# Kernel tuning notes

Measured on AMD Instinct MI355X. Metric: run time of the kernel, lower is better.

The kernel has to match this reference:

```python
import jax, jax.numpy as jnp
import numpy as np

_SCAN_CHUNK = 32


def _causal_decay_scan(x, decay, init):
    """Inclusive scan out[t] = decay*out[t-1] + x[t], chunked closed form.
    x: [B,H,T,D], decay: [1,H,1], init: [B,H,D]. Returns [B,H,T,D]."""
    B, H, T, D = x.shape
    C = min(_SCAN_CHUNK, T)
    assert T % C == 0
    nC = T // C
    log_decay = jnp.log(jnp.clip(decay.astype(jnp.float32), 1e-8, None))  # [1,H,1]
    c_idx = jnp.arange(C, dtype=jnp.float32)
    log_p = log_decay[..., None] * c_idx.reshape(1, 1, C, 1)              # [1,H,C,1]
    p = jnp.exp(log_p)
    inv_p = jnp.exp(-log_p)
    init_p = jnp.exp(log_decay[..., None] * (c_idx + 1.0).reshape(1, 1, C, 1))
    # [nC, B, H, C, D] so lax.scan chains chunk states causally
    xc = x.reshape(B, H, nC, C, D).transpose(2, 0, 1, 3, 4).astype(jnp.float32)

    def step(state, chunk):  # state [B,H,D], chunk [B,H,C,D]
        cs = jnp.cumsum(chunk * inv_p, axis=2)
        out = cs * p + state[:, :, None, :] * init_p
        return out[:, :, -1, :], out

    _, outs = jax.lax.scan(step, init.astype(jnp.float32), xc)
    return outs.transpose(1, 2, 0, 3, 4).reshape(B, H, T, D).astype(x.dtype)


def _phi(x):
    return jax.nn.elu(x) + 1.0


def setup_inputs() -> dict:
    key = jax.random.key(0)
    ks = jax.random.split(key, 5)
    B, T, hidden, H = 4, 4096, 1024, 16
    s = 1.0 / np.sqrt(hidden)
    x = jax.random.normal(ks[0], (B, T, hidden), dtype=jnp.float32)
    Wqkv = jax.random.normal(ks[1], (3 * hidden, hidden), dtype=jnp.float32) * s
    Wout = jax.random.normal(ks[2], (hidden, hidden), dtype=jnp.float32) * s
    Wgate = jax.random.normal(ks[3], (hidden, hidden), dtype=jnp.float32) * s
    bgate = jnp.zeros((hidden,), dtype=jnp.float32)
    logit = float(np.log(0.95 / 0.05))  # sigmoid(logit) == 0.95
    decay_param = jnp.full((H,), logit, dtype=jnp.float32)
    return {"x": x, "Wqkv": Wqkv, "Wout": Wout, "Wgate": Wgate,
            "bgate": bgate, "decay_param": decay_param}


def reference(x, Wqkv, Wout, Wgate, bgate, decay_param):
    B, T, hidden = x.shape
    H = decay_param.shape[0]
    D = hidden // H
    qkv = x @ Wqkv.T                       # [B,T,3*hidden]
    q, k, v = jnp.split(qkv, 3, axis=-1)
    # [B,T,hidden] -> [B,H,T,D]
    q = q.reshape(B, T, H, D).transpose(0, 2, 1, 3)
    k = k.reshape(B, T, H, D).transpose(0, 2, 1, 3)
    v = v.reshape(B, T, H, D).transpose(0, 2, 1, 3)
    q = _phi(q)
    k = _phi(k)
    decay = jax.nn.sigmoid(decay_param).reshape(1, H, 1)
    kv_init = jnp.zeros((B, H, D), dtype=x.dtype)
    ksum_init = jnp.zeros((B, H, D), dtype=x.dtype)
    running_kv = _causal_decay_scan(k * v, decay, kv_init)
    running_ksum = _causal_decay_scan(k, decay, ksum_init)
    den = jnp.clip(jnp.sum(q * running_ksum, axis=-1, keepdims=True), 1e-6, None)
    out = q * running_kv / den             # [B,H,T,D]
    v_direct = v.transpose(0, 2, 1, 3).reshape(B, T, hidden)
    out = out.transpose(0, 2, 1, 3).reshape(B, T, hidden)
    g = jax.nn.sigmoid(out @ Wgate.T + bgate)
    out = g * out + (1.0 - g) * v_direct
    return out @ Wout.T
```

## Files before the change

### kernel.cpp

```cpp
#include <hip/hip_runtime.h>

typedef unsigned short u16;
typedef __bf16 bf16x8 __attribute__((ext_vector_type(8)));
typedef float f32x4 __attribute__((ext_vector_type(4)));

#define BB 4
#define TT 4096
#define HID 1024
#define NH 16
#define HD 64
#define BT (BB*TT)
#define NCH 128
#define LOG_NCH 7
#define CLEN (TT/NCH)

__device__ __forceinline__ float bf2f(u16 u) {
    return __uint_as_float(((unsigned)u) << 16);
}
__device__ __forceinline__ u16 f2bf(float f) {
    unsigned u = __float_as_uint(f);
    unsigned r = 0x7FFFu + ((u >> 16) & 1u);
    return (u16)((u + r) >> 16);
}
__device__ __forceinline__ float phi(float x) {
    return x > 0.f ? x + 1.f : __expf(x);
}
__device__ __forceinline__ float sigmoidf(float x) {
    return 1.f / (1.f + __expf(-x));
}
__device__ __forceinline__ float4 u4_to_f4(ushort4 u) {
    return make_float4(bf2f(u.x), bf2f(u.y), bf2f(u.z), bf2f(u.w));
}

#define CN1 (BT*HID/4)
#define CN2 (3*HID*HID/4)
#define CN3 (HID*HID/4)
#define CN4 (HID*HID/4)
__global__ void convert_all(const float4* __restrict__ x,    const float4* __restrict__ wqkv,
                            const float4* __restrict__ wgate, const float4* __restrict__ wout,
                            ushort4* __restrict__ xb,    ushort4* __restrict__ wqkvb,
                            ushort4* __restrict__ wgateb, ushort4* __restrict__ woutb) {
    int i = blockIdx.x * 256 + threadIdx.x;
    const float4* src; ushort4* dst; int j;
    if (i < CN1)                 { src = x;     dst = xb;     j = i; }
    else if (i < CN1+CN2)        { src = wqkv;  dst = wqkvb;  j = i - CN1; }
    else if (i < CN1+CN2+CN3)    { src = wgate; dst = wgateb; j = i - CN1 - CN2; }
    else                         { src = wout;  dst = woutb;  j = i - CN1 - CN2 - CN3; }
    float4 f = src[j];
    ushort4 u;
    u.x = f2bf(f.x); u.y = f2bf(f.y); u.z = f2bf(f.z); u.w = f2bf(f.w);
    dst[j] = u;
}

template<int EPI>
__global__ __launch_bounds__(512, 2)
void gemm256(const u16* __restrict__ A, const u16* __restrict__ Bm,
             int M, int N, int K, void* __restrict__ Cout,
             const float* __restrict__ bg,
             const u16* __restrict__ attn,
             const u16* __restrict__ qkv)
{
    __shared__ u16 As[2][256 * 64];
    __shared__ u16 Bs[2][256 * 64];
    const int tid  = threadIdx.x;
    const int wave = tid >> 6;
    const int lane = tid & 63;
    const int r16  = lane & 15;
    const int m0 = blockIdx.y * 256;
    const int n0 = blockIdx.x * 256;
    const int wm = (wave & 1) * 128;
    const int wn = (wave >> 1) * 64;

    f32x4 acc[8][4];
    #pragma unroll
    for (int i = 0; i < 8; ++i)
        #pragma unroll
        for (int j = 0; j < 4; ++j)
            acc[i][j] = (f32x4){0.f, 0.f, 0.f, 0.f};

    auto STAGE = [&](int k0, int buf) {
        #pragma unroll
        for (int j = 0; j < 4; ++j) {
            int s   = j * 8 + wave;
            int idx = s * 64 + lane;
            int pr  = idx >> 3;
            int lc  = (idx & 7) ^ (pr & 7);
            const u16* gA = A  + (size_t)(m0 + pr) * K + k0 + lc * 8;
            const u16* gB = Bm + (size_t)(n0 + pr) * K + k0 + lc * 8;
            __builtin_amdgcn_global_load_lds(
                (const __attribute__((address_space(1))) void*)gA,
                (__attribute__((address_space(3))) void*)&As[buf][s * 512], 16, 0, 0);
            __builtin_amdgcn_global_load_lds(
                (const __attribute__((address_space(1))) void*)gB,
                (__attribute__((address_space(3))) void*)&Bs[buf][s * 512], 16, 0, 0);
        }
    };

    auto COMPUTE = [&](int buf) {
        bf16x8 bq[4][2];
        #pragma unroll
        for (int j = 0; j < 4; ++j) {
            #pragma unroll
            for (int ks = 0; ks < 2; ++ks) {
                int lcq = ks * 4 + (lane >> 4);
                int pcq = lcq ^ (r16 & 7);
                bq[j][ks] = *(const bf16x8*)&Bs[buf][(wn + j * 16 + r16) * 64 + pcq * 8];
            }
        }
        #pragma unroll
        for (int rh = 0; rh < 2; ++rh) {
            bf16x8 af[4][2];
            #pragma unroll
            for (int i = 0; i < 4; ++i) {
                #pragma unroll
                for (int ks = 0; ks < 2; ++ks) {
                    int lcq = ks * 4 + (lane >> 4);
                    int pcq = lcq ^ (r16 & 7);
                    af[i][ks] = *(const bf16x8*)&As[buf][(wm + rh * 64 + i * 16 + r16) * 64 + pcq * 8];
                }
            }
            __builtin_amdgcn_s_setprio(1);
            #pragma unroll
            for (int i = 0; i < 4; ++i)
                #pragma unroll
                for (int j = 0; j < 4; ++j)
                    #pragma unroll
                    for (int ks = 0; ks < 2; ++ks)
                        acc[rh * 4 + i][j] = __builtin_amdgcn_mfma_f32_16x16x32_bf16(
                            af[i][ks], bq[j][ks], acc[rh * 4 + i][j], 0, 0, 0);
            __builtin_amdgcn_s_setprio(0);
        }
    };

    const int nt = K >> 6;
    STAGE(0, 0);
    STAGE(64, 1);
    asm volatile("s_waitcnt vmcnt(8)" ::: "memory");
    __builtin_amdgcn_sched_barrier(0);
    __builtin_amdgcn_s_barrier();
    __builtin_amdgcn_sched_barrier(0);

    for (int t = 0; t < nt; ++t) {
        COMPUTE(t & 1);
        if (t + 1 < nt) {
            __builtin_amdgcn_sched_barrier(0);
            __builtin_amdgcn_s_barrier();
            __builtin_amdgcn_sched_barrier(0);
            if (t + 2 < nt) {
                STAGE((t + 2) << 6, t & 1);
                asm volatile("s_waitcnt vmcnt(8)" ::: "memory");
            } else {
                asm volatile("s_waitcnt vmcnt(0)" ::: "memory");
            }
            __builtin_amdgcn_sched_barrier(0);
            __builtin_amdgcn_s_barrier();
            __builtin_amdgcn_sched_barrier(0);
        }
    }

    #pragma unroll
    for (int rh = 0; rh < 2; ++rh) {
        #pragma unroll
        for (int i = 0; i < 4; ++i) {
            int rowb = m0 + wm + rh * 64 + i * 16 + (lane >> 4) * 4;
            #pragma unroll
            for (int j = 0; j < 4; ++j) {
                int col = n0 + wn + j * 16 + r16;
                #pragma unroll
                for (int r = 0; r < 4; ++r) {
                    float v = acc[rh * 4 + i][j][r];
                    size_t row = (size_t)(rowb + r);
                    if (EPI == 0) {
                        ((u16*)Cout)[row * N + col] = f2bf(v);
                    } else if (EPI == 1) {
                        float g  = sigmoidf(v + bg[col]);
                        float at = bf2f(attn[row * HID + col]);
                        float vd = bf2f(qkv[row * (3 * HID) + 2 * HID + col]);
                        ((u16*)Cout)[row * HID + col] = f2bf(g * at + (1.f - g) * vd);
                    } else {
                        ((float*)Cout)[row * N + col] = v;
                    }
                }
            }
        }
    }
}

__global__ void scan_finals(const u16* __restrict__ qkv, const float* __restrict__ decay_param,
                            float* __restrict__ ckv, float* __restrict__ cks) {
    int g  = blockIdx.x * 16 + (threadIdx.x >> 4);
    int sl = threadIdx.x & 15;
    int c = g & (NCH - 1);
    int h = (g >> LOG_NCH) & (NH - 1);
    int b = g >> (LOG_NCH + 4);
    float decay = sigmoidf(decay_param[h]);
    const u16* kp = qkv + (size_t)(b * TT + c * CLEN) * (3 * HID) + HID + h * HD + sl * 4;
    float4 skv = make_float4(0.f, 0.f, 0.f, 0.f);
    float4 sks = make_float4(0.f, 0.f, 0.f, 0.f);
    for (int t = 0; t < CLEN; ++t) {
        float4 k = u4_to_f4(*(const ushort4*)kp);
        float4 v = u4_to_f4(*(const ushort4*)(kp + HID));
        k.x = phi(k.x); k.y = phi(k.y); k.z = phi(k.z); k.w = phi(k.w);
        skv.x = decay * skv.x + k.x * v.x;  skv.y = decay * skv.y + k.y * v.y;
        skv.z = decay * skv.z + k.z * v.z;  skv.w = decay * skv.w + k.w * v.w;
        sks.x = decay * sks.x + k.x;        sks.y = decay * sks.y + k.y;
        sks.z = decay * sks.z + k.z;        sks.w = decay * sks.w + k.w;
        kp += 3 * HID;
    }
    *(float4*)(ckv + (size_t)g * 64 + sl * 4) = skv;
    *(float4*)(cks + (size_t)g * 64 + sl * 4) = sks;
}

__global__ void scan_prefix(float* __restrict__ ckv, float* __restrict__ cks,
                            const float* __restrict__ decay_param) {
    int bh = blockIdx.x;
    int h  = bh & (NH - 1);
    int lane = threadIdx.x;
    float decay = sigmoidf(decay_param[h]);
    float dC = powf(decay, (float)CLEN);
    float* pkv = ckv + (size_t)bh * NCH * 64 + lane;
    float* pks = cks + (size_t)bh * NCH * 64 + lane;
    float fkv = 0.f, fks = 0.f;
    for (int c = 0; c < NCH; ++c) {
        float lkv = pkv[c * 64], lks = pks[c * 64];
        pkv[c * 64] = fkv; pks[c * 64] = fks;
        fkv = fkv * dC + lkv;
        fks = fks * dC + lks;
    }
}

__global__ void scan_apply(const u16* __restrict__ qkv, const float* __restrict__ decay_param,
                           const float* __restrict__ ckv, const float* __restrict__ cks,
                           u16* __restrict__ attn) {
    int g  = blockIdx.x * 16 + (threadIdx.x >> 4);
    int sl = threadIdx.x & 15;
    int c = g & (NCH - 1);
    int h = (g >> LOG_NCH) & (NH - 1);
    int b = g >> (LOG_NCH + 4);
    float decay = sigmoidf(decay_param[h]);
    float4 skv = *(const float4*)(ckv + (size_t)g * 64 + sl * 4);
    float4 sks = *(const float4*)(cks + (size_t)g * 64 + sl * 4);
    const u16* qp = qkv + (size_t)(b * TT + c * CLEN) * (3 * HID) + h * HD + sl * 4;
    u16* op = attn + (size_t)(b * TT + c * CLEN) * HID + h * HD + sl * 4;
    for (int t = 0; t < CLEN; ++t) {
        float4 q = u4_to_f4(*(const ushort4*)qp);
        float4 k = u4_to_f4(*(const ushort4*)(qp + HID));
        float4 v = u4_to_f4(*(const ushort4*)(qp + 2 * HID));
        q.x = phi(q.x); q.y = phi(q.y); q.z = phi(q.z); q.w = phi(q.w);
        k.x = phi(k.x); k.y = phi(k.y); k.z = phi(k.z); k.w = phi(k.w);
        skv.x = decay * skv.x + k.x * v.x;  skv.y = decay * skv.y + k.y * v.y;
        skv.z = decay * skv.z + k.z * v.z;  skv.w = decay * skv.w + k.w * v.w;
        sks.x = decay * sks.x + k.x;        sks.y = decay * sks.y + k.y;
        sks.z = decay * sks.z + k.z;        sks.w = decay * sks.w + k.w;
        float s = q.x * sks.x + q.y * sks.y + q.z * sks.z + q.w * sks.w;
        s += __shfl_xor(s, 8);
        s += __shfl_xor(s, 4);
        s += __shfl_xor(s, 2);
        s += __shfl_xor(s, 1);
        float inv = 1.f / fmaxf(s, 1e-6f);
        ushort4 o;
        o.x = f2bf(q.x * skv.x * inv); o.y = f2bf(q.y * skv.y * inv);
        o.z = f2bf(q.z * skv.z * inv); o.w = f2bf(q.w * skv.w * inv);
        *(ushort4*)op = o;
        qp += 3 * HID;
        op += HID;
    }
}

extern "C" void kernel_launch(void* const* d_in, const int* in_sizes, int n_in,
                              void* d_out, int out_size, void* d_ws, size_t ws_size,
                              hipStream_t stream) {
    const float* x     = (const float*)d_in[0];
    const float* Wqkv  = (const float*)d_in[1];
    const float* Wout  = (const float*)d_in[2];
    const float* Wgate = (const float*)d_in[3];
    const float* bgate = (const float*)d_in[4];
    const float* decay = (const float*)d_in[5];

    u16* xb     = (u16*)d_ws;
    u16* wqkvb  = xb    + (size_t)BT * HID;
    u16* wgateb = wqkvb + (size_t)3 * HID * HID;
    u16* woutb  = wgateb + (size_t)HID * HID;
    u16* qkvb   = woutb + (size_t)HID * HID;
    u16* out2b  = qkvb  + (size_t)BT * 3 * HID;
    float* ckv  = (float*)(out2b + (size_t)BT * HID);
    float* cks  = ckv + (size_t)BB * NH * NCH * HD;
    u16* attnb  = xb;

    convert_all<<<(CN1 + CN2 + CN3 + CN4) / 256, 256, 0, stream>>>(
        (const float4*)x, (const float4*)Wqkv, (const float4*)Wgate, (const float4*)Wout,
        (ushort4*)xb, (ushort4*)wqkvb, (ushort4*)wgateb, (ushort4*)woutb);

    gemm256<0><<<dim3(3 * HID / 256, BT / 256), 512, 0, stream>>>(
        xb, wqkvb, BT, 3 * HID, HID, qkvb, nullptr, nullptr, nullptr);

    scan_finals<<<BB * NH * NCH / 16, 256, 0, stream>>>(qkvb, decay, ckv, cks);
    scan_prefix<<<BB * NH, 64, 0, stream>>>(ckv, cks, decay);
    scan_apply<<<BB * NH * NCH / 16, 256, 0, stream>>>(qkvb, decay, ckv, cks, attnb);

    gemm256<1><<<dim3(HID / 256, BT / 256), 512, 0, stream>>>(
        attnb, wgateb, BT, HID, HID, out2b, bgate, attnb, qkvb);

    gemm256<2><<<dim3(HID / 256, BT / 256), 512, 0, stream>>>(
        out2b, woutb, BT, HID, HID, d_out, nullptr, nullptr, nullptr);
}
```

Before: 376.8 us.

## Restructure GEMM main loop into 8-phase quadrant-interleaved load/MFMA schedule

```diff
diff --git a/kernel.cpp b/kernel.cpp
--- a/kernel.cpp
+++ b/kernel.cpp
@@ -78,112 +78,153 @@
         for (int j = 0; j < 4; ++j)
             acc[i][j] = (f32x4){0.f, 0.f, 0.f, 0.f};
 
-    auto STAGE = [&](int k0, int buf) {
+    bf16x8 af[4][2];
+    bf16x8 bq[2][2];
+
+    auto STAGE_A = [&](int k0, int buf, int mq) {
         #pragma unroll
-        for (int j = 0; j < 4; ++j) {
-            int s   = j * 8 + wave;
-            int idx = s * 64 + lane;
-            int pr  = idx >> 3;
-            int lc  = (idx & 7) ^ (pr & 7);
-            const u16* gA = A  + (size_t)(m0 + pr) * K + k0 + lc * 8;
-            const u16* gB = Bm + (size_t)(n0 + pr) * K + k0 + lc * 8;
+        for (int l = 0; l < 2; ++l) {
+            int q    = wave * 2 + l;
+            int row0 = (q >> 3) * 128 + mq * 64 + (q & 7) * 8;
+            int row  = row0 + (lane >> 3);
+            int lc   = (lane & 7) ^ (row & 7);
+            const u16* g = A + (size_t)(m0 + row) * K + k0 + lc * 8;
             __builtin_amdgcn_global_load_lds(
-                (const __attribute__((address_space(1))) void*)gA,
-                (__attribute__((address_space(3))) void*)&As[buf][s * 512], 16, 0, 0);
-            __builtin_amdgcn_global_load_lds(
-                (const __attribute__((address_space(1))) void*)gB,
-                (__attribute__((address_space(3))) void*)&Bs[buf][s * 512], 16, 0, 0);
+                (const __attribute__((address_space(1))) void*)g,
+                (__attribute__((address_space(3))) void*)&As[buf][row0 * 64], 16, 0, 0);
         }
     };
-
-    auto COMPUTE = [&](int buf) {
-        bf16x8 bq[4][2];
+    auto STAGE_B = [&](int k0, int buf, int nq) {
         #pragma unroll
-        for (int j = 0; j < 4; ++j) {
-            #pragma unroll
-            for (int ks = 0; ks < 2; ++ks) {
-                int lcq = ks * 4 + (lane >> 4);
-                int pcq = lcq ^ (r16 & 7);
-                bq[j][ks] = *(const bf16x8*)&Bs[buf][(wn + j * 16 + r16) * 64 + pcq * 8];
-            }
-        }
-        #pragma unroll
-        for (int rh = 0; rh < 2; ++rh) {
-            bf16x8 af[4][2];
-            #pragma unroll
-            for (int i = 0; i < 4; ++i) {
-                #pragma unroll
-                for (int ks = 0; ks < 2; ++ks) {
-                    int lcq = ks * 4 + (lane >> 4);
-                    int pcq = lcq ^ (r16 & 7);
-                    af[i][ks] = *(const bf16x8*)&As[buf][(wm + rh * 64 + i * 16 + r16) * 64 + pcq * 8];
-                }
-            }
-            __builtin_amdgcn_s_setprio(1);
-            #pragma unroll
-            for (int i = 0; i < 4; ++i)
-                #pragma unroll
-                for (int j = 0; j < 4; ++j)
-                    #pragma unroll
-                    for (int ks = 0; ks < 2; ++ks)
-                        acc[rh * 4 + i][j] = __builtin_amdgcn_mfma_f32_16x16x32_bf16(
-                            af[i][ks], bq[j][ks], acc[rh * 4 + i][j], 0, 0, 0);
-            __builtin_amdgcn_s_setprio(0);
+        for (int l = 0; l < 2; ++l) {
+            int q    = wave * 2 + l;
+            int row0 = (q >> 2) * 64 + nq * 32 + (q & 3) * 8;
+            int row  = row0 + (lane >> 3);
+            int lc   = (lane & 7) ^ (row & 7);
+            const u16* g = Bm + (size_t)(n0 + row) * K + k0 + lc * 8;
+            __builtin_amdgcn_global_load_lds(
+                (const __attribute__((address_space(1))) void*)g,
+                (__attribute__((address_space(3))) void*)&Bs[buf][row0 * 64], 16, 0, 0);
         }
     };
 
-    const int nt = K >> 6;
-    STAGE(0, 0);
-    STAGE(64, 1);
-    asm volatile("s_waitcnt vmcnt(8)" ::: "memory");
-    __builtin_amdgcn_sched_barrier(0);
-    __builtin_amdgcn_s_barrier();
-    __builtin_amdgcn_sched_barrier(0);
-
-    for (int t = 0; t < nt; ++t) {
-        COMPUTE(t & 1);
-        if (t + 1 < nt) {
-            __builtin_amdgcn_sched_barrier(0);
-            __builtin_amdgcn_s_barrier();
-            __builtin_amdgcn_sched_barrier(0);
-            if (t + 2 < nt) {
-                STAGE((t + 2) << 6, t & 1);
-                asm volatile("s_waitcnt vmcnt(8)" ::: "memory");
-            } else {
-                asm volatile("s_waitcnt vmcnt(0)" ::: "memory");
-            }
-            __builtin_amdgcn_sched_barrier(0);
-            __builtin_amdgcn_s_barrier();
-            __builtin_amdgcn_sched_barrier(0);
-        }
+#define DS_A(BUF, MQ)                                                          \
+    _Pragma("unroll") for (int i_ = 0; i_ < 4; ++i_)                           \
+    _Pragma("unroll") for (int ks_ = 0; ks_ < 2; ++ks_) {                      \
+        int pcq = (ks_ * 4 + (lane >> 4)) ^ (r16 & 7);                         \
+        af[i_][ks_] = *(const bf16x8*)                                         \
+            &As[BUF][(wm + (MQ) * 64 + i_ * 16 + r16) * 64 + pcq * 8];         \
+    }
+#define DS_B(BUF, NQ)                                                          \
+    _Pragma("unroll") for (int j_ = 0; j_ < 2; ++j_)                           \
+    _Pragma("unroll") for (int ks_ = 0; ks_ < 2; ++ks_) {                      \
+        int pcq = (ks_ * 4 + (lane >> 4)) ^ (r16 & 7);                         \
+        bq[j_][ks_] = *(const bf16x8*)                                         \
+            &Bs[BUF][(wn + (NQ) * 32 + j_ * 16 + r16) * 64 + pcq * 8];         \
+    }
+#define MFMA_Q(MQ, NQ)                                                         \
+    __builtin_amdgcn_s_setprio(1);                                             \
+    _Pragma("unroll") for (int i_ = 0; i_ < 4; ++i_)                           \
+    _Pragma("unroll") for (int j_ = 0; j_ < 2; ++j_)                           \
+    _Pragma("unroll") for (int ks_ = 0; ks_ < 2; ++ks_)                        \
+        acc[(MQ) * 4 + i_][(NQ) * 2 + j_] =                                    \
+            __builtin_amdgcn_mfma_f32_16x16x32_bf16(                           \
+                af[i_][ks_], bq[j_][ks_], acc[(MQ) * 4 + i_][(NQ) * 2 + j_],   \
+                0, 0, 0);                                                      \
+    __builtin_amdgcn_s_setprio(0);
+#define SB __builtin_amdgcn_sched_barrier(0)
+#define PH_MID  SB; __builtin_amdgcn_s_barrier();                              \
+                asm volatile("s_waitcnt lgkmcnt(0)" ::: "memory"); SB;
+#define PH_END  SB; __builtin_amdgcn_s_barrier(); SB;
+#define PH_END_VM(N)  SB; asm volatile("s_waitcnt vmcnt(" #N ")" ::: "memory");\
+                __builtin_amdgcn_s_barrier(); SB;
+
+    const int niter = K >> 7;
+
+    STAGE_A(0, 0, 0); STAGE_B(0, 0, 0); STAGE_A(0, 0, 1); STAGE_B(0, 0, 1);
+    STAGE_B(64, 1, 0); STAGE_A(64, 1, 1);
+    PH_END_VM(4);
+
+    for (int i = 0; i < niter - 1; ++i) {
+        const int kb = i * 128;
+        DS_A(0, 0) DS_B(0, 0)
+        STAGE_A(kb + 64, 1, 0);
+        PH_MID; MFMA_Q(0, 0); PH_END;
+        DS_A(0, 1)
+        STAGE_B(kb + 64, 1, 1);
+        PH_MID; MFMA_Q(1, 0); PH_END;
+        DS_B(0, 1)
+        STAGE_B(kb + 128, 0, 0);
+        PH_MID; MFMA_Q(1, 1); PH_END;
+        DS_A(0, 0)
+        STAGE_A(kb + 128, 0, 1);
+        PH_MID; MFMA_Q(0, 1); PH_END_VM(4);
+        DS_A(1, 0) DS_B(1, 0)
+        STAGE_A(kb + 128, 0, 0);
+        PH_MID; MFMA_Q(0, 0); PH_END;
+        DS_A(1, 1)
+        STAGE_B(kb + 128, 0, 1);
+        PH_MID; MFMA_Q(1, 0); PH_END;
+        DS_B(1, 1)
+        STAGE_B(kb + 192, 1, 0);
+        PH_MID; MFMA_Q(1, 1); PH_END;
+        DS_A(1, 0)
+        STAGE_A(kb + 192, 1, 1);
+        PH_MID; MFMA_Q(0, 1); PH_END_VM(4);
+    }
+
+    {
+        const int kb = (niter - 1) * 128;
+        DS_A(0, 0) DS_B(0, 0)
+        STAGE_A(kb + 64, 1, 0);
+        PH_MID; MFMA_Q(0, 0); PH_END;
+        DS_A(0, 1)
+        STAGE_B(kb + 64, 1, 1);
+        PH_MID; MFMA_Q(1, 0); PH_END;
+        DS_B(0, 1)
+        PH_MID; MFMA_Q(1, 1); PH_END;
+        DS_A(0, 0)
+        PH_MID; MFMA_Q(0, 1); PH_END_VM(0);
+        DS_A(1, 0) DS_B(1, 0)
+        PH_MID; MFMA_Q(0, 0); PH_END;
+        DS_A(1, 1)
+        PH_MID; MFMA_Q(1, 0); PH_END;
+        DS_B(1, 1)
+        PH_MID; MFMA_Q(1, 1); PH_END;
+        DS_A(1, 0)
+        PH_MID; MFMA_Q(0, 1); PH_END;
     }
 
     #pragma unroll
-    for (int rh = 0; rh < 2; ++rh) {
+    for (int mi = 0; mi < 8; ++mi) {
+        int rowb = m0 + wm + mi * 16 + (lane >> 4) * 4;
         #pragma unroll
-        for (int i = 0; i < 4; ++i) {
-            int rowb = m0 + wm + rh * 64 + i * 16 + (lane >> 4) * 4;
+        for (int nj = 0; nj < 4; ++nj) {
+            int col = n0 + wn + nj * 16 + r16;
             #pragma unroll
-            for (int j = 0; j < 4; ++j) {
-                int col = n0 + wn + j * 16 + r16;
-                #pragma unroll
-                for (int r = 0; r < 4; ++r) {
-                    float v = acc[rh * 4 + i][j][r];
-                    size_t row = (size_t)(rowb + r);
-                    if (EPI == 0) {
-                        ((u16*)Cout)[row * N + col] = f2bf(v);
-                    } else if (EPI == 1) {
-                        float g  = sigmoidf(v + bg[col]);
-                        float at = bf2f(attn[row * HID + col]);
-                        float vd = bf2f(qkv[row * (3 * HID) + 2 * HID + col]);
-                        ((u16*)Cout)[row * HID + col] = f2bf(g * at + (1.f - g) * vd);
-                    } else {
-                        ((float*)Cout)[row * N + col] = v;
-                    }
+            for (int r = 0; r < 4; ++r) {
+                float v = acc[mi][nj][r];
+                size_t row = (size_t)(rowb + r);
+                if (EPI == 0) {
+                    ((u16*)Cout)[row * N + col] = f2bf(v);
+                } else if (EPI == 1) {
+                    float g  = sigmoidf(v + bg[col]);
+                    float at = bf2f(attn[row * HID + col]);
+                    float vd = bf2f(qkv[row * (3 * HID) + 2 * HID + col]);
+                    ((u16*)Cout)[row * HID + col] = f2bf(g * at + (1.f - g) * vd);
+                } else {
+                    ((float*)Cout)[row * N + col] = v;
                 }
             }
         }
     }
+#undef DS_A
+#undef DS_B
+#undef MFMA_Q
+#undef SB
+#undef PH_MID
+#undef PH_END
+#undef PH_END_VM
 }
 
 __global__ void scan_finals(const u16* __restrict__ qkv, const float* __restrict__ decay_param,
```

Result: slower. 387.0 us (+2.7%).

## Use 128x128 single-buffered GEMM kernel for QKV projection

Applied to the files above, without the earlier changes.

```diff
diff --git a/kernel.cpp b/kernel.cpp
--- a/kernel.cpp
+++ b/kernel.cpp
@@ -50,6 +50,95 @@
     ushort4 u;
     u.x = f2bf(f.x); u.y = f2bf(f.y); u.z = f2bf(f.z); u.w = f2bf(f.w);
     dst[j] = u;
+}
+
+template<int EPI>
+__global__ __launch_bounds__(256)
+void gemm_bt(const u16* __restrict__ A, const u16* __restrict__ Bm,
+             int M, int N, int K, void* __restrict__ Cout,
+             const float* __restrict__ bg,
+             const u16* __restrict__ attn,
+             const u16* __restrict__ qkv)
+{
+    __shared__ u16 As[128 * 64];
+    __shared__ u16 Bs[128 * 64];
+    const int tid  = threadIdx.x;
+    const int wave = tid >> 6;
+    const int lane = tid & 63;
+    const int m0 = blockIdx.y * 128;
+    const int n0 = blockIdx.x * 128;
+    const int mw = (wave & 1) * 64;
+    const int nw = (wave >> 1) * 64;
+    const int r16 = lane & 15;
+
+    f32x4 acc[4][4];
+    #pragma unroll
+    for (int i = 0; i < 4; ++i)
+        #pragma unroll
+        for (int j = 0; j < 4; ++j)
+            acc[i][j] = (f32x4){0.f, 0.f, 0.f, 0.f};
+
+    for (int k0 = 0; k0 < K; k0 += 64) {
+        #pragma unroll
+        for (int i = 0; i < 4; ++i) {
+            int s   = i * 4 + wave;
+            int idx = s * 64 + lane;
+            int pr  = idx >> 3;
+            int pc  = idx & 7;
+            int lc  = pc ^ (pr & 7);
+            const u16* gA = A  + (size_t)(m0 + pr) * K + k0 + lc * 8;
+            const u16* gB = Bm + (size_t)(n0 + pr) * K + k0 + lc * 8;
+            __builtin_amdgcn_global_load_lds(
+                (const __attribute__((address_space(1))) void*)gA,
+                (__attribute__((address_space(3))) void*)&As[s * 512], 16, 0, 0);
+            __builtin_amdgcn_global_load_lds(
+                (const __attribute__((address_space(1))) void*)gB,
+                (__attribute__((address_space(3))) void*)&Bs[s * 512], 16, 0, 0);
+        }
+        __syncthreads();
+        #pragma unroll
+        for (int s2 = 0; s2 < 2; ++s2) {
+            const int lcq = s2 * 4 + (lane >> 4);
+            const int pcq = lcq ^ (r16 & 7);
+            bf16x8 af[4], bq[4];
+            #pragma unroll
+            for (int i = 0; i < 4; ++i)
+                af[i] = *(const bf16x8*)&As[(mw + i * 16 + r16) * 64 + pcq * 8];
+            #pragma unroll
+            for (int j = 0; j < 4; ++j)
+                bq[j] = *(const bf16x8*)&Bs[(nw + j * 16 + r16) * 64 + pcq * 8];
+            #pragma unroll
+            for (int i = 0; i < 4; ++i)
+                #pragma unroll
+                for (int j = 0; j < 4; ++j)
+                    acc[i][j] = __builtin_amdgcn_mfma_f32_16x16x32_bf16(af[i], bq[j], acc[i][j], 0, 0, 0);
+        }
+        __syncthreads();
+    }
+
+    #pragma unroll
+    for (int i = 0; i < 4; ++i) {
+        int rowb = m0 + mw + i * 16 + (lane >> 4) * 4;
+        #pragma unroll
+        for (int j = 0; j < 4; ++j) {
+            int col = n0 + nw + j * 16 + r16;
+            #pragma unroll
+            for (int r = 0; r < 4; ++r) {
+                float v = acc[i][j][r];
+                size_t row = (size_t)(rowb + r);
+                if (EPI == 0) {
+                    ((u16*)Cout)[row * N + col] = f2bf(v);
+                } else if (EPI == 1) {
+                    float g  = sigmoidf(v + bg[col]);
+                    float at = bf2f(attn[row * HID + col]);
+                    float vd = bf2f(qkv[row * (3 * HID) + 2 * HID + col]);
+                    ((u16*)Cout)[row * HID + col] = f2bf(g * at + (1.f - g) * vd);
+                } else {
+                    ((float*)Cout)[row * N + col] = v;
+                }
+            }
+        }
+    }
 }
 
 template<int EPI>
@@ -291,7 +380,7 @@
         (const float4*)x, (const float4*)Wqkv, (const float4*)Wgate, (const float4*)Wout,
         (ushort4*)xb, (ushort4*)wqkvb, (ushort4*)wgateb, (ushort4*)woutb);
 
-    gemm256<0><<<dim3(3 * HID / 256, BT / 256), 512, 0, stream>>>(
+    gemm_bt<0><<<dim3(3 * HID / 128, BT / 128), 256, 0, stream>>>(
         xb, wqkvb, BT, 3 * HID, HID, qkvb, nullptr, nullptr, nullptr);
 
     scan_finals<<<BB * NH * NCH / 16, 256, 0, stream>>>(qkvb, decay, ckv, cks);
```

New measurement: 384.7 us, median of 2. 2.1% more time.
